# Optimization experiments

Measured on AMD Instinct MI355X. Metric: run time of the kernel, lower is better.

The kernel has to match this reference:

```python
import jax, jax.numpy as jnp
import numpy as np
from jax import lax

N, M, D, K = 65536, 16, 128, 8
DD = D // K  # delta_d


def _normalize(x, axis):
    # torch F.normalize: x / max(||x||_2, 1e-12)
    return x / jnp.maximum(jnp.linalg.norm(x, axis=axis, keepdims=True), 1e-12)


def setup_inputs() -> dict:
    key0 = jax.random.key(0)
    k1, k2, k3, k4 = jax.random.split(key0, 4)
    h = jax.random.normal(k1, (N, D), dtype=jnp.float32)
    neighbors = jax.random.randint(k2, (N * M,), 0, N)
    stdv = 1.0 / np.sqrt(DD)
    query = jax.random.uniform(k3, (DD, DD), minval=-stdv, maxval=stdv, dtype=jnp.float32)
    key_w = jax.random.uniform(k4, (DD, DD), minval=-stdv, maxval=stdv, dtype=jnp.float32)
    return {"h": h, "neighbors": neighbors, "query": query, "key_w": key_w,
            "iterat": 3, "max_iter": 10}


def _calc_prob(x, centre, cov):
    # x: [n,1,dd], centre: [n,k,dd], cov: [n,k,dd]
    dd = centre.shape[-1]
    diff = x - centre  # [n,k,dd]
    log_result = jnp.log(cov)
    log_result = jnp.where(jnp.isnan(log_result), jnp.float32(1e-6), log_result)
    # double-log as in the original (may produce NaN for negative log_result)
    dets = jnp.exp(jnp.sum(jnp.log(log_result), axis=2))  # [n,k]
    coef = jnp.float32(1.0 / np.sqrt((2.0 * np.pi) ** dd / 2.0))
    left = coef / jnp.sqrt(dets + 1e-6)  # [n,k]
    # diff @ diag(cov) @ diff^T == sum(cov * diff^2)
    right = jnp.exp(-0.5 * jnp.sum(cov * diff * diff, axis=2))  # [n,k]
    prob = left * right
    prob = _normalize(prob, axis=1)
    prob = jnp.where(jnp.isnan(prob), jnp.float32(1e-6), prob)
    return prob


def _forward(h, neighbors, query, key_w, iterat):
    n, d = h.shape
    dd = query.shape[0]
    k = d // dd
    m = neighbors.shape[0] // n
    nb = h[neighbors].reshape(n, m, k, dd)  # neighbor gather [n,m,k,dd]
    hc = _normalize(h.reshape(n, k, dd), axis=2)  # per-capsule normalized [n,k,dd]
    q = jnp.einsum('nke,ef->nkf', hc, query)
    kk = jnp.einsum('nke,ef->nkf', hc, key_w)
    # diagonal of q @ kk^T over capsules
    att_logit = jnp.einsum('nke,nke->nk', q, kk)
    att = jax.nn.softmax(att_logit, axis=1)[..., None]  # [n,k,1]

    # ---- calcCovs (no grad in original) ----
    qs = jnp.einsum('nmke,ef->nmkf', nb, query)  # [n,m,k,dd]
    # sum over neighbors of (qs @ kk^T): [n,k,k]
    p_matrix = jnp.einsum('nmkf,njf->nkj', qs, kk)
    diagv = jnp.diagonal(p_matrix, axis1=1, axis2=2)  # [n,k]
    # torch quirk: p[i] = torch.diag(p_matrix[i]) broadcasts the diag vector across rows
    p_b = jnp.broadcast_to(diagv[:, None, :], (n, k, k))
    sub = jnp.concatenate([nb, hc[:, None]], axis=1)  # [n,m+1,k,dd]
    sub = jnp.transpose(sub, (0, 2, 1, 3))  # [n,k,m+1,dd]
    sub = _normalize(sub, axis=2)  # normalize along neighbor axis
    L = m + 1
    # torch.median returns the lower median -> sorted element at (L-1)//2
    middle = jnp.sort(sub, axis=2)[:, :, (L - 1) // 2, :]  # [n,k,dd]
    cov = jnp.einsum('nij,njd->nid', p_b, (hc - middle) ** 2)  # [n,k,dd]
    cov = lax.stop_gradient(cov)

    # ---- iterative routing ----
    ix = jnp.sum(att * hc, axis=1, keepdims=True)  # [n,1,dd]
    for _ in range(iterat):
        p = lax.stop_gradient(_calc_prob(ix, hc, cov))[..., None]  # [n,k,1]
        ix = jnp.sum(att * p * hc, axis=1, keepdims=True) / (
            jnp.sum(att * p, axis=1, keepdims=True) + 1e-9)
    x = _normalize(ix[:, 0, :], axis=1)  # [n,dd]
    return x, att[..., 0]


def reference(h, neighbors, query, key_w, iterat, max_iter):
    del max_iter  # unused in the original forward
    return _forward(h, neighbors, query, key_w, iterat)
```

## Files before the change

### kernel.cpp

```cpp
#include <hip/hip_runtime.h>
#include <hip/hip_bf16.h>

#define MD 128
#define KC 8
#define KD 16
#define MN 16
#define QS 20

typedef _Float16 f16x2 __attribute__((ext_vector_type(2)));

static __device__ __forceinline__ float lo_bf(unsigned int w){ union{unsigned int i;float f;}c; c.i=w<<16;        return c.f; }
static __device__ __forceinline__ float hi_bf(unsigned int w){ union{unsigned int i;float f;}c; c.i=w&0xffff0000u; return c.f; }
static __device__ __forceinline__ float bf2f1(unsigned short u){ union{unsigned int i;float f;}c; c.i=((unsigned int)u)<<16; return c.f; }

template<bool BF>
static __device__ __forceinline__ float load1(const void* base, int off) {
    if (BF) return bf2f1(((const unsigned short*)base)[off]);
    return ((const float*)base)[off];
}

static __device__ __forceinline__ float fast_rsq(float x){ return __builtin_amdgcn_rsqf(x); }
static __device__ __forceinline__ float fast_rcp(float x){ return __builtin_amdgcn_rcpf(x); }

template<int CTRL>
static __device__ __forceinline__ float dpp_mov(float v) {
    return __int_as_float(__builtin_amdgcn_update_dpp(
        0, __float_as_int(v), CTRL, 0xF, 0xF, true));
}

static __device__ __forceinline__ float rsum_quad(float v) {
    v += dpp_mov<0xB1>(v);
    v += dpp_mov<0x4E>(v);
    return v;
}
static __device__ __forceinline__ float rsum_caps(float v) {
    v += dpp_mov<0x124>(v);
    v += dpp_mov<0x128>(v);
    v += __shfl_xor(v, 16);
    return v;
}
static __device__ __forceinline__ float rmax_caps(float v) {
    v = fmaxf(v, dpp_mov<0x124>(v));
    v = fmaxf(v, dpp_mov<0x128>(v));
    v = fmaxf(v, __shfl_xor(v, 16));
    return v;
}

static __device__ __forceinline__ unsigned phmin(unsigned a, unsigned b) {
    return __builtin_bit_cast(unsigned, __builtin_elementwise_min(
        __builtin_bit_cast(f16x2, a), __builtin_bit_cast(f16x2, b)));
}
static __device__ __forceinline__ unsigned phmax(unsigned a, unsigned b) {
    return __builtin_bit_cast(unsigned, __builtin_elementwise_max(
        __builtin_bit_cast(f16x2, a), __builtin_bit_cast(f16x2, b)));
}
static __device__ __forceinline__ void pcas(unsigned& x, unsigned& y) {
    unsigned lo = phmin(x, y), hi = phmax(x, y); x = lo; y = hi;
}
static __device__ __forceinline__ void psort8(unsigned a[8]) {
    pcas(a[0],a[1]); pcas(a[2],a[3]); pcas(a[4],a[5]); pcas(a[6],a[7]);
    pcas(a[0],a[2]); pcas(a[1],a[3]); pcas(a[4],a[6]); pcas(a[5],a[7]);
    pcas(a[1],a[2]); pcas(a[5],a[6]);
    pcas(a[0],a[4]); pcas(a[2],a[6]); pcas(a[2],a[4]);
    pcas(a[1],a[5]); pcas(a[3],a[7]); pcas(a[3],a[5]);
    pcas(a[1],a[2]); pcas(a[3],a[4]); pcas(a[5],a[6]);
}
static __device__ __forceinline__ void pmed16(unsigned a[16], unsigned& b7, unsigned& b8) {
    psort8(a); psort8(a + 8);
    const unsigned* u = a; const unsigned* v = a + 8;
    unsigned t7 =             phmin(u[7], v[0]);
    t7 = phmax(t7, phmin(u[6], v[1]));
    t7 = phmax(t7, phmin(u[5], v[2]));
    t7 = phmax(t7, phmin(u[4], v[3]));
    t7 = phmax(t7, phmin(u[3], v[4]));
    t7 = phmax(t7, phmin(u[2], v[5]));
    t7 = phmax(t7, phmin(u[1], v[6]));
    t7 = phmax(t7, phmin(u[0], v[7]));
    unsigned t8 = phmax(u[0], v[0]);
    t8 = phmax(t8, phmin(u[7], v[1]));
    t8 = phmax(t8, phmin(u[6], v[2]));
    t8 = phmax(t8, phmin(u[5], v[3]));
    t8 = phmax(t8, phmin(u[4], v[4]));
    t8 = phmax(t8, phmin(u[3], v[5]));
    t8 = phmax(t8, phmin(u[2], v[6]));
    t8 = phmax(t8, phmin(u[1], v[7]));
    b7 = t7; b8 = t8;
}

static __device__ __forceinline__ void cas(float& x, float& y) {
    float lo = fminf(x, y), hi = fmaxf(x, y); x = lo; y = hi;
}
static __device__ __forceinline__ void sort8f(float a[8]) {
    cas(a[0],a[1]); cas(a[2],a[3]); cas(a[4],a[5]); cas(a[6],a[7]);
    cas(a[0],a[2]); cas(a[1],a[3]); cas(a[4],a[6]); cas(a[5],a[7]);
    cas(a[1],a[2]); cas(a[5],a[6]);
    cas(a[0],a[4]); cas(a[2],a[6]); cas(a[2],a[4]);
    cas(a[1],a[5]); cas(a[3],a[7]); cas(a[3],a[5]);
    cas(a[1],a[2]); cas(a[3],a[4]); cas(a[5],a[6]);
}
static __device__ __forceinline__ float med17f(float a[16], float self) {
    sort8f(a); sort8f(a + 8);
    const float* u = a; const float* v = a + 8;
    float t7 =            fminf(u[7], v[0]);
    t7 = fmaxf(t7, fminf(u[6], v[1])); t7 = fmaxf(t7, fminf(u[5], v[2]));
    t7 = fmaxf(t7, fminf(u[4], v[3])); t7 = fmaxf(t7, fminf(u[3], v[4]));
    t7 = fmaxf(t7, fminf(u[2], v[5])); t7 = fmaxf(t7, fminf(u[1], v[6]));
    t7 = fmaxf(t7, fminf(u[0], v[7]));
    float t8 = fmaxf(u[0], v[0]);
    t8 = fmaxf(t8, fminf(u[7], v[1])); t8 = fmaxf(t8, fminf(u[6], v[2]));
    t8 = fmaxf(t8, fminf(u[5], v[3])); t8 = fmaxf(t8, fminf(u[4], v[4]));
    t8 = fmaxf(t8, fminf(u[3], v[5])); t8 = fmaxf(t8, fminf(u[2], v[6]));
    t8 = fmaxf(t8, fminf(u[1], v[7]));
    return __builtin_amdgcn_fmed3f(self, t7, t8);
}

template<bool BF>
__global__ __launch_bounds__(256)
void attn_fwd(const void* __restrict__ hraw,
              const int* __restrict__ nbr,
              const void* __restrict__ qry,
              const void* __restrict__ keyw,
              const int* __restrict__ iterat_p,
              void* __restrict__ out,
              int n_nodes)
{
    const int tid  = threadIdx.x;
    const int wid  = tid >> 6;
    const int l    = tid & 63;
    const int sub  = l & 31;
    const int half = (l >> 5) & 1;
    const int k    = sub >> 2;
    const int q4   = sub & 3;

    const int iterat = iterat_p[0];

    {
        uint2 w = ((const uint2*)hraw)[l];
        float a0 = fabsf(lo_bf(w.x)); a0 = (a0 != a0) ? 1e30f : a0;
        float a1 = fabsf(hi_bf(w.x)); a1 = (a1 != a1) ? 1e30f : a1;
        float a2 = fabsf(lo_bf(w.y)); a2 = (a2 != a2) ? 1e30f : a2;
        float a3 = fabsf(hi_bf(w.y)); a3 = (a3 != a3) ? 1e30f : a3;
        float m = fmaxf(fmaxf(a0, a1), fmaxf(a2, a3));
        m = fmaxf(m, dpp_mov<0xB1>(m));
        m = fmaxf(m, dpp_mov<0x4E>(m));
        m = fmaxf(m, dpp_mov<0x124>(m));
        m = fmaxf(m, dpp_mov<0x128>(m));
        m = fmaxf(m, __shfl_xor(m, 16));
        m = fmaxf(m, __shfl_xor(m, 32));
        if ((m < 1000.0f) != BF) return;
    }

    int n = blockIdx.x * 8 + wid * 2 + half;
    if (n >= n_nodes) n = n_nodes - 1;

    __shared__ float qs[16 * QS];
    __shared__ float kts[16 * QS];
    {
        float qv = load1<BF>(qry, tid);
        float kv = load1<BF>(keyw, tid);
        int e = tid >> 4, f = tid & 15;
        qs [e * QS + f] = qv;
        kts[f * QS + e] = kv;
    }

    int nnb = blockIdx.x * 8 + wid * 2 + ((l >> 4) & 1);
    if (nnb >= n_nodes) nnb = n_nodes - 1;
    const int nbv = nbr[nnb * MN + (l & 15)];

    float hp[4];
    if (BF) {
        uint2 w0 = ((const uint2*)hraw)[(size_t)n * 32 + sub];
        hp[0] = lo_bf(w0.x); hp[1] = hi_bf(w0.x); hp[2] = lo_bf(w0.y); hp[3] = hi_bf(w0.y);
    } else {
        float4 t = ((const float4*)hraw)[(size_t)n * 32 + sub];
        hp[0] = t.x; hp[1] = t.y; hp[2] = t.z; hp[3] = t.w;
    }
    float ss = 0;
    #pragma unroll
    for (int i = 0; i < 4; ++i) ss = fmaf(hp[i], hp[i], ss);
    ss = rsum_quad(ss);
    float inv = fast_rsq(fmaxf(ss, 1e-24f));
    float hc[4];
    #pragma unroll
    for (int i = 0; i < 4; ++i) hc[i] = hp[i] * inv;

    __syncthreads();

    const int vb = half << 6;
    unsigned rbx[16], rby[16]; float4 rf[16];
    #pragma unroll
    for (int m = 0; m < MN; ++m) {
        int idx = __builtin_amdgcn_ds_bpermute(vb + m * 4, nbv);
        if (BF) {
            uint2 t = *(const uint2*)((const char*)hraw + (((unsigned)idx << 8) + (unsigned)sub * 8u));
            rbx[m] = t.x; rby[m] = t.y;
        } else {
            rf[m] = *(const float4*)((const char*)hraw + (((unsigned)idx << 9) + (unsigned)sub * 16u));
        }
    }

    float hcA[4][4];
    #pragma unroll
    for (int j = 0; j < 4; ++j) {
        hcA[0][j] = dpp_mov<0x00>(hc[j]);
        hcA[1][j] = dpp_mov<0x55>(hc[j]);
        hcA[2][j] = dpp_mov<0xAA>(hc[j]);
        hcA[3][j] = dpp_mov<0xFF>(hc[j]);
    }
    float kk[4];
    #pragma unroll
    for (int i = 0; i < 4; ++i) {
        const float* row = &kts[(q4 * 4 + i) * QS];
        float acc = 0;
        #pragma unroll
        for (int r = 0; r < 4; ++r) {
            float4 kr = *(const float4*)(row + r * 4);
            acc = fmaf(hcA[r][0], kr.x, acc);
            acc = fmaf(hcA[r][1], kr.y, acc);
            acc = fmaf(hcA[r][2], kr.z, acc);
            acc = fmaf(hcA[r][3], kr.w, acc);
        }
        kk[i] = acc;
    }
    float kkA[4][4];
    #pragma unroll
    for (int j = 0; j < 4; ++j) {
        kkA[0][j] = dpp_mov<0x00>(kk[j]);
        kkA[1][j] = dpp_mov<0x55>(kk[j]);
        kkA[2][j] = dpp_mov<0xAA>(kk[j]);
        kkA[3][j] = dpp_mov<0xFF>(kk[j]);
    }
    float w[4];
    #pragma unroll
    for (int i = 0; i < 4; ++i) {
        const float* row = &qs[(q4 * 4 + i) * QS];
        float acc = 0;
        #pragma unroll
        for (int r = 0; r < 4; ++r) {
            float4 qr = *(const float4*)(row + r * 4);
            acc = fmaf(kkA[r][0], qr.x, acc);
            acc = fmaf(kkA[r][1], qr.y, acc);
            acc = fmaf(kkA[r][2], qr.z, acc);
            acc = fmaf(kkA[r][3], qr.w, acc);
        }
        w[i] = acc;
    }

    float lg = 0;
    #pragma unroll
    for (int i = 0; i < 4; ++i) lg = fmaf(hc[i], w[i], lg);
    float logit = rsum_quad(lg);
    float mx  = rmax_caps(logit);
    float ex  = __expf(logit - mx);
    float att = ex * fast_rcp(rsum_caps(ex));

    float sn[4] = {0,0,0,0}, s2[4] = {0,0,0,0};
    #pragma unroll
    for (int m = 0; m < 16; ++m) {
        float x0, x1, x2, x3;
        if (BF) { x0=lo_bf(rbx[m]); x1=hi_bf(rbx[m]); x2=lo_bf(rby[m]); x3=hi_bf(rby[m]); }
        else    { x0=rf[m].x; x1=rf[m].y; x2=rf[m].z; x3=rf[m].w; }
        sn[0]+=x0; sn[1]+=x1; sn[2]+=x2; sn[3]+=x3;
        s2[0]=fmaf(x0,x0,s2[0]); s2[1]=fmaf(x1,x1,s2[1]);
        s2[2]=fmaf(x2,x2,s2[2]); s2[3]=fmaf(x3,x3,s2[3]);
    }

    float mid[4];
    if (BF) {
        unsigned b7, b8;
        pmed16(rbx, b7, b8);
        mid[0] = __builtin_amdgcn_fmed3f(hc[0], lo_bf(b7), lo_bf(b8));
        mid[1] = __builtin_amdgcn_fmed3f(hc[1], hi_bf(b7), hi_bf(b8));
        pmed16(rby, b7, b8);
        mid[2] = __builtin_amdgcn_fmed3f(hc[2], lo_bf(b7), lo_bf(b8));
        mid[3] = __builtin_amdgcn_fmed3f(hc[3], hi_bf(b7), hi_bf(b8));
    } else {
        #pragma unroll
        for (int c = 0; c < 4; ++c) {
            float a[16];
            #pragma unroll
            for (int m = 0; m < 16; ++m)
                a[m] = (c==0) ? rf[m].x : (c==1) ? rf[m].y : (c==2) ? rf[m].z : rf[m].w;
            mid[c] = med17f(a, hc[c]);
        }
    }
    #pragma unroll
    for (int c = 0; c < 4; ++c) {
        float t2 = fmaf(hc[c], hc[c], s2[c]);
        mid[c] *= fast_rsq(fmaxf(t2, 1e-24f));
    }

    float dgl = 0;
    #pragma unroll
    for (int i = 0; i < 4; ++i) dgl = fmaf(sn[i], w[i], dgl);
    float dg = rsum_quad(dgl);

    float cv[4];
    #pragma unroll
    for (int i = 0; i < 4; ++i) {
        float t = hc[i] - mid[i];
        cv[i] = rsum_caps(dg * t * t);
    }

    float lsl = 0;
    #pragma unroll
    for (int i = 0; i < 4; ++i) {
        float lr = __logf(cv[i]);
        lr = (lr != lr) ? 1e-6f : lr;
        lsl += __logf(lr);
    }
    float ls   = rsum_quad(lsl);
    float dets = __expf(ls);
    const float coef = 5.822108e-7f;
    float left = coef * fast_rsq(dets + 1e-6f);

    float ah[4], ix[4];
    #pragma unroll
    for (int i = 0; i < 4; ++i) ah[i] = att * hc[i];
    #pragma unroll
    for (int i = 0; i < 4; ++i) ix[i] = rsum_caps(ah[i]);

    for (int it = 0; it < iterat; ++it) {
        float rsl = 0;
        #pragma unroll
        for (int i = 0; i < 4; ++i) {
            float df = ix[i] - hc[i];
            rsl = fmaf(cv[i] * df, df, rsl);
        }
        float rs   = rsum_quad(rsl);
        float prob = left * __expf(-0.5f * rs);
        float p2   = rsum_caps(prob * prob);
        float pn   = prob * fast_rsq(fmaxf(p2, 1e-24f));
        pn = (pn != pn) ? 1e-6f : pn;
        float den = rsum_caps(att * pn);
        float num[4];
        #pragma unroll
        for (int i = 0; i < 4; ++i) num[i] = rsum_caps(pn * ah[i]);
        float rr = fast_rcp(den + 1e-9f);
        #pragma unroll
        for (int i = 0; i < 4; ++i) ix[i] = num[i] * rr;
    }

    float xs = 0;
    #pragma unroll
    for (int i = 0; i < 4; ++i) xs = fmaf(ix[i], ix[i], xs);
    xs = rsum_quad(xs);
    float xinv = fast_rsq(fmaxf(xs, 1e-24f));

    if (BF) {
        if (sub < 4) {
            __hip_bfloat16 b0 = __float2bfloat16(ix[0] * xinv);
            __hip_bfloat16 b1 = __float2bfloat16(ix[1] * xinv);
            __hip_bfloat16 b2 = __float2bfloat16(ix[2] * xinv);
            __hip_bfloat16 b3 = __float2bfloat16(ix[3] * xinv);
            uint2 o;
            o.x = (unsigned)(*(unsigned short*)&b0) | ((unsigned)(*(unsigned short*)&b1) << 16);
            o.y = (unsigned)(*(unsigned short*)&b2) | ((unsigned)(*(unsigned short*)&b3) << 16);
            *(uint2*)((char*)out + (size_t)n * 32 + q4 * 8) = o;
        }
        if (q4 == 0) {
            __hip_bfloat16 ba = __float2bfloat16(att);
            ((unsigned short*)out)[(size_t)n_nodes * KD + (size_t)n * KC + k] =
                *(unsigned short*)&ba;
        }
    } else {
        if (sub < 4) {
            float4 o;
            o.x = ix[0] * xinv; o.y = ix[1] * xinv; o.z = ix[2] * xinv; o.w = ix[3] * xinv;
            *(float4*)((float*)out + (size_t)n * KD + q4 * 4) = o;
        }
        if (q4 == 0) ((float*)out)[(size_t)n_nodes * KD + (size_t)n * KC + k] = att;
    }
}

extern "C" void kernel_launch(void* const* d_in, const int* in_sizes, int n_in,
                              void* d_out, int out_size, void* d_ws, size_t ws_size,
                              hipStream_t stream) {
    const void* h    = d_in[0];
    const int*  nbr  = (const int*)d_in[1];
    const void* qry  = d_in[2];
    const void* keyw = (const void*)d_in[3];
    const int*  iterat_p = (const int*)d_in[4];

    int n_nodes = in_sizes[0] / MD;

    int blocks = (n_nodes + 7) / 8;
    attn_fwd<true ><<<blocks, 256, 0, stream>>>(h, nbr, qry, keyw, iterat_p, d_out, n_nodes);
    attn_fwd<false><<<blocks, 256, 0, stream>>>(h, nbr, qry, keyw, iterat_p, d_out, n_nodes);
}
```

Before: 88.40 us.

## Precompute query·keyᵀ product matrix once and detect dtype in a setup kernel

Adds a tiny setup kernel that computes the 16x16 matrix Q·Kᵀ and the bf16/fp32 format flag into workspace. The main kernel loads this matrix into shared memory and does one matrix-vector product per capsule instead of two, and it also drops the per-block dtype probe reduction. This saves ALU and DPP work and lets the h load be issued before the early-exit check. In exchange it adds a third launch and a global read of a workspace flag, and the reassociated product can change rounding slightly.

```diff
diff --git a/kernel.cpp b/kernel.cpp
--- a/kernel.cpp
+++ b/kernel.cpp
@@ -12,12 +12,6 @@
 static __device__ __forceinline__ float lo_bf(unsigned int w){ union{unsigned int i;float f;}c; c.i=w<<16;        return c.f; }
 static __device__ __forceinline__ float hi_bf(unsigned int w){ union{unsigned int i;float f;}c; c.i=w&0xffff0000u; return c.f; }
 static __device__ __forceinline__ float bf2f1(unsigned short u){ union{unsigned int i;float f;}c; c.i=((unsigned int)u)<<16; return c.f; }
-
-template<bool BF>
-static __device__ __forceinline__ float load1(const void* base, int off) {
-    if (BF) return bf2f1(((const unsigned short*)base)[off]);
-    return ((const float*)base)[off];
-}
 
 static __device__ __forceinline__ float fast_rsq(float x){ return __builtin_amdgcn_rsqf(x); }
 static __device__ __forceinline__ float fast_rcp(float x){ return __builtin_amdgcn_rcpf(x); }
@@ -114,12 +108,49 @@
     return __builtin_amdgcn_fmed3f(self, t7, t8);
 }
 
+__global__ void setup_m(const void* __restrict__ hraw,
+                        const void* __restrict__ qry,
+                        const void* __restrict__ keyw,
+                        void* __restrict__ ws)
+{
+    const int tid = threadIdx.x;
+    unsigned w = ((const unsigned*)hraw)[tid];
+    float a0 = fabsf(lo_bf(w)); a0 = (a0 != a0) ? 1e30f : a0;
+    float a1 = fabsf(hi_bf(w)); a1 = (a1 != a1) ? 1e30f : a1;
+    float m = fmaxf(a0, a1);
+    m = fmaxf(m, dpp_mov<0xB1>(m));
+    m = fmaxf(m, dpp_mov<0x4E>(m));
+    m = fmaxf(m, dpp_mov<0x124>(m));
+    m = fmaxf(m, dpp_mov<0x128>(m));
+    m = fmaxf(m, __shfl_xor(m, 16));
+    m = fmaxf(m, __shfl_xor(m, 32));
+    const bool isbf = (m < 1000.0f);
+
+    const int e = tid >> 4, g = tid & 15;
+    float acc = 0.f;
+    if (isbf) {
+        const unsigned short* q  = (const unsigned short*)qry;
+        const unsigned short* kw = (const unsigned short*)keyw;
+        #pragma unroll
+        for (int f = 0; f < 16; ++f)
+            acc = fmaf(bf2f1(q[e * 16 + f]), bf2f1(kw[g * 16 + f]), acc);
+    } else {
+        const float* q  = (const float*)qry;
+        const float* kw = (const float*)keyw;
+        #pragma unroll
+        for (int f = 0; f < 16; ++f)
+            acc = fmaf(q[e * 16 + f], kw[g * 16 + f], acc);
+    }
+    ((float*)((char*)ws + 64))[tid] = acc;
+    if (tid == 0) ((int*)ws)[0] = isbf ? 1 : 0;
+}
+
 template<bool BF>
 __global__ __launch_bounds__(256)
 void attn_fwd(const void* __restrict__ hraw,
               const int* __restrict__ nbr,
-              const void* __restrict__ qry,
-              const void* __restrict__ keyw,
+              const float* __restrict__ Mws,
+              const int* __restrict__ flagp,
               const int* __restrict__ iterat_p,
               void* __restrict__ out,
               int n_nodes)
@@ -132,49 +163,28 @@
     const int k    = sub >> 2;
     const int q4   = sub & 3;
 
-    const int iterat = iterat_p[0];
-
-    {
-        uint2 w = ((const uint2*)hraw)[l];
-        float a0 = fabsf(lo_bf(w.x)); a0 = (a0 != a0) ? 1e30f : a0;
-        float a1 = fabsf(hi_bf(w.x)); a1 = (a1 != a1) ? 1e30f : a1;
-        float a2 = fabsf(lo_bf(w.y)); a2 = (a2 != a2) ? 1e30f : a2;
-        float a3 = fabsf(hi_bf(w.y)); a3 = (a3 != a3) ? 1e30f : a3;
-        float m = fmaxf(fmaxf(a0, a1), fmaxf(a2, a3));
-        m = fmaxf(m, dpp_mov<0xB1>(m));
-        m = fmaxf(m, dpp_mov<0x4E>(m));
-        m = fmaxf(m, dpp_mov<0x124>(m));
-        m = fmaxf(m, dpp_mov<0x128>(m));
-        m = fmaxf(m, __shfl_xor(m, 16));
-        m = fmaxf(m, __shfl_xor(m, 32));
-        if ((m < 1000.0f) != BF) return;
-    }
-
     int n = blockIdx.x * 8 + wid * 2 + half;
     if (n >= n_nodes) n = n_nodes - 1;
-
-    __shared__ float qs[16 * QS];
-    __shared__ float kts[16 * QS];
-    {
-        float qv = load1<BF>(qry, tid);
-        float kv = load1<BF>(keyw, tid);
-        int e = tid >> 4, f = tid & 15;
-        qs [e * QS + f] = qv;
-        kts[f * QS + e] = kv;
-    }
 
     int nnb = blockIdx.x * 8 + wid * 2 + ((l >> 4) & 1);
     if (nnb >= n_nodes) nnb = n_nodes - 1;
     const int nbv = nbr[nnb * MN + (l & 15)];
 
+    uint2 hp_b; float4 hp_f;
+    if (BF) hp_b = ((const uint2*)hraw)[(size_t)n * 32 + sub];
+    else    hp_f = ((const float4*)hraw)[(size_t)n * 32 + sub];
+
+    const float mval = Mws[tid];
+    const int iterat = iterat_p[0];
+
+    if ((flagp[0] == 1) != BF) return;
+
+    __shared__ float ms[16 * QS];
+    ms[(tid >> 4) * QS + (tid & 15)] = mval;
+
     float hp[4];
-    if (BF) {
-        uint2 w0 = ((const uint2*)hraw)[(size_t)n * 32 + sub];
-        hp[0] = lo_bf(w0.x); hp[1] = hi_bf(w0.x); hp[2] = lo_bf(w0.y); hp[3] = hi_bf(w0.y);
-    } else {
-        float4 t = ((const float4*)hraw)[(size_t)n * 32 + sub];
-        hp[0] = t.x; hp[1] = t.y; hp[2] = t.z; hp[3] = t.w;
-    }
+    if (BF) { hp[0]=lo_bf(hp_b.x); hp[1]=hi_bf(hp_b.x); hp[2]=lo_bf(hp_b.y); hp[3]=hi_bf(hp_b.y); }
+    else    { hp[0]=hp_f.x; hp[1]=hp_f.y; hp[2]=hp_f.z; hp[3]=hp_f.w; }
     float ss = 0;
     #pragma unroll
     for (int i = 0; i < 4; ++i) ss = fmaf(hp[i], hp[i], ss);
@@ -207,41 +217,18 @@
         hcA[2][j] = dpp_mov<0xAA>(hc[j]);
         hcA[3][j] = dpp_mov<0xFF>(hc[j]);
     }
-    float kk[4];
+    float w[4];
     #pragma unroll
     for (int i = 0; i < 4; ++i) {
-        const float* row = &kts[(q4 * 4 + i) * QS];
+        const float* row = &ms[(q4 * 4 + i) * QS];
         float acc = 0;
         #pragma unroll
         for (int r = 0; r < 4; ++r) {
-            float4 kr = *(const float4*)(row + r * 4);
-            acc = fmaf(hcA[r][0], kr.x, acc);
-            acc = fmaf(hcA[r][1], kr.y, acc);
-            acc = fmaf(hcA[r][2], kr.z, acc);
-            acc = fmaf(hcA[r][3], kr.w, acc);
-        }
-        kk[i] = acc;
-    }
-    float kkA[4][4];
-    #pragma unroll
-    for (int j = 0; j < 4; ++j) {
-        kkA[0][j] = dpp_mov<0x00>(kk[j]);
-        kkA[1][j] = dpp_mov<0x55>(kk[j]);
-        kkA[2][j] = dpp_mov<0xAA>(kk[j]);
-        kkA[3][j] = dpp_mov<0xFF>(kk[j]);
-    }
-    float w[4];
-    #pragma unroll
-    for (int i = 0; i < 4; ++i) {
-        const float* row = &qs[(q4 * 4 + i) * QS];
-        float acc = 0;
-        #pragma unroll
-        for (int r = 0; r < 4; ++r) {
-            float4 qr = *(const float4*)(row + r * 4);
-            acc = fmaf(kkA[r][0], qr.x, acc);
-            acc = fmaf(kkA[r][1], qr.y, acc);
-            acc = fmaf(kkA[r][2], qr.z, acc);
-            acc = fmaf(kkA[r][3], qr.w, acc);
+            float4 mr = *(const float4*)(row + r * 4);
+            acc = fmaf(hcA[r][0], mr.x, acc);
+            acc = fmaf(hcA[r][1], mr.y, acc);
+            acc = fmaf(hcA[r][2], mr.z, acc);
+            acc = fmaf(hcA[r][3], mr.w, acc);
         }
         w[i] = acc;
     }
@@ -384,7 +371,12 @@
 
     int n_nodes = in_sizes[0] / MD;
 
+    const int*   flag = (const int*)d_ws;
+    const float* M    = (const float*)((char*)d_ws + 64);
+
+    setup_m<<<1, 256, 0, stream>>>(h, qry, keyw, d_ws);
+
     int blocks = (n_nodes + 7) / 8;
-    attn_fwd<true ><<<blocks, 256, 0, stream>>>(h, nbr, qry, keyw, iterat_p, d_out, n_nodes);
-    attn_fwd<false><<<blocks, 256, 0, stream>>>(h, nbr, qry, keyw, iterat_p, d_out, n_nodes);
-}
+    attn_fwd<true ><<<blocks, 256, 0, stream>>>(h, nbr, M, flag, iterat_p, d_out, n_nodes);
+    attn_fwd<false><<<blocks, 256, 0, stream>>>(h, nbr, M, flag, iterat_p, d_out, n_nodes);
+}
```

After: 84.90 us. 3.9% less time.
